# Performance work log

Hardware: AMD Instinct MI355X
Metric: run time of the kernel (lower is better)

## Reference

```python
import jax, jax.numpy as jnp
import numpy as np

B, S, D_IN, D_OUT = 4, 4096, 2048, 2048
DELTA_A = 0.0
DELTA_W = 0.05


def setup_inputs() -> dict:
    key = jax.random.key(0)
    kx, kw = jax.random.split(key)
    # xavier_uniform bound for [out, in] weight
    bound = float(np.sqrt(6.0 / (D_IN + D_OUT)))
    x = jax.random.normal(kx, (B, S, D_IN), dtype=jnp.float32)
    W = jax.random.uniform(kw, (D_OUT, D_IN), dtype=jnp.float32, minval=-bound, maxval=bound)
    b = jnp.zeros((D_OUT,), dtype=jnp.float32)
    return {"x": x, "W": W, "b": b}


def reference(x, W, b):
    # --- activation ternarization (BitNet STE); pre_ln=False -> identity ---
    ax = jnp.abs(x)
    thr_a = DELTA_A * jnp.mean(ax, axis=-1, keepdims=True)
    xa = jnp.where(ax < thr_a, jnp.zeros_like(x), jnp.sign(x))
    x_final = x + jax.lax.stop_gradient(xa - x)

    # --- weight ternarization with per-row alpha scale ---
    Wc = W - jnp.mean(W, axis=1, keepdims=True)
    aWc = jnp.abs(Wc)
    thr_w = DELTA_W * jnp.mean(aWc, axis=1, keepdims=True)
    code = jnp.where(aWc < thr_w, jnp.zeros_like(Wc), jnp.sign(Wc))
    nz = (code != 0).astype(Wc.dtype)
    alpha = jnp.sum(aWc * nz, axis=1, keepdims=True) / jnp.clip(
        jnp.sum(nz, axis=1, keepdims=True), 1.0, None
    )
    Wq = alpha * code
    W_final = W + jax.lax.stop_gradient(Wq - W)

    # F.linear: y = x @ W^T + b
    return jnp.einsum("bsd,od->bso", x_final, W_final) + b
```

## Files before the change

### kernel.cpp

```cpp
#include <hip/hip_runtime.h>
#include <stdint.h>

#define K_DIM   2048
#define N_DIM   2048
#define M_DIM   16384
#define DELTA_W 0.05f

#define BM 256
#define BN 256
#define BK 128
#define NT (K_DIM / BK)

typedef __attribute__((ext_vector_type(4))) int i32x4;

__device__ __forceinline__ void async_copy16(const void* g, void* l) {
    __builtin_amdgcn_global_load_lds(
        (__attribute__((address_space(1))) void*)g,
        (__attribute__((address_space(3))) void*)l,
        16, 0, 0);
}

__device__ __forceinline__ float block_sum_256(float v, float* sm) {
#pragma unroll
    for (int o = 32; o > 0; o >>= 1) v += __shfl_down(v, o, 64);
    const int lane = threadIdx.x & 63;
    const int w    = threadIdx.x >> 6;
    __syncthreads();
    if (lane == 0) sm[w] = v;
    __syncthreads();
    return sm[0] + sm[1] + sm[2] + sm[3];
}

__global__ __launch_bounds__(256) void quant_kernel(
    const float* __restrict__ W, const float* __restrict__ x,
    int8_t* __restrict__ code, float* __restrict__ alpha,
    int8_t* __restrict__ xq)
{
    __shared__ float sm[4];
    const int t = threadIdx.x;

    if (blockIdx.x < N_DIM) {
        const int row = blockIdx.x;
        const float* Wr = W + (size_t)row * K_DIM;

        float v[8];
        float s = 0.f;
#pragma unroll
        for (int i = 0; i < 8; ++i) { v[i] = Wr[t + i * 256]; s += v[i]; }
        const float mean = block_sum_256(s, sm) * (1.0f / K_DIM);

        float sa = 0.f;
#pragma unroll
        for (int i = 0; i < 8; ++i) sa += fabsf(v[i] - mean);
        const float thr = DELTA_W * (block_sum_256(sa, sm) * (1.0f / K_DIM));

        float ssum = 0.f, scnt = 0.f;
        int8_t q[8];
#pragma unroll
        for (int i = 0; i < 8; ++i) {
            const float c = v[i] - mean;
            const float a = fabsf(c);
            int8_t qv = 0;
            if (a >= thr) qv = (int8_t)((c > 0.f) - (c < 0.f));
            q[i] = qv;
            if (qv != 0) { ssum += a; scnt += 1.0f; }
        }
        const float num = block_sum_256(ssum, sm);
        const float den = block_sum_256(scnt, sm);
        if (t == 0) alpha[row] = num / fmaxf(den, 1.0f);

#pragma unroll
        for (int i = 0; i < 8; ++i)
            code[(size_t)row * K_DIM + t + i * 256] = q[i];
    } else {
        const int blk = blockIdx.x - N_DIM;
        const int base = blk * 1024 + t;
        const float4* xin = (const float4*)x;
        char4* xo = (char4*)xq;
#pragma unroll
        for (int i = 0; i < 4; ++i) {
            const float4 f = xin[base + i * 256];
            char4 c;
            c.x = (char)((f.x > 0.f) - (f.x < 0.f));
            c.y = (char)((f.y > 0.f) - (f.y < 0.f));
            c.z = (char)((f.z > 0.f) - (f.z < 0.f));
            c.w = (char)((f.w > 0.f) - (f.w < 0.f));
            xo[base + i * 256] = c;
        }
    }
}

__global__ __launch_bounds__(512) void gemm_kernel(
    const int8_t* __restrict__ A, const int8_t* __restrict__ Bt,
    const float* __restrict__ alpha, const float* __restrict__ bias,
    float* __restrict__ out)
{
    __shared__ __align__(16) int8_t As[2][BM * BK];
    __shared__ __align__(16) int8_t Bs[2][BN * BK];

    const int tid  = threadIdx.x;
    const int lane = tid & 63;
    const int wv   = tid >> 6;
    const int wm   = (wv >> 2) * 128;
    const int wn   = (wv & 3) * 64;
    const int fr   = lane & 15;
    const int q    = lane >> 4;
    const int c0   = q ^ (fr & 7);

    const int tileM = blockIdx.y * BM;
    const int tileN = blockIdx.x * BN;

    size_t a_src[2][2], b_src[2][2];
#pragma unroll
    for (int e = 0; e < 2; ++e) {
        const int s  = e * 512 + tid;
        const int r  = s >> 3;
        const int cg = (s & 7) ^ (r & 7);
#pragma unroll
        for (int h = 0; h < 2; ++h) {
            a_src[h][e] = (size_t)(tileM + h * 128 + r) * K_DIM + cg * 16;
            b_src[h][e] = (size_t)(tileN + h * 128 + r) * K_DIM + cg * 16;
        }
    }

    i32x4 acc[8][4] = {};
    i32x4 af[2][4], bf0[2][2], bf1[2][2];

#define STAGE_A(nbp, h, kk0) do {                                              \
    async_copy16(A  + a_src[h][0] + (kk0), &As[nbp][(h) * 16384 + tid * 16]);  \
    async_copy16(A  + a_src[h][1] + (kk0),                                     \
                 &As[nbp][(h) * 16384 + 8192 + tid * 16]);                     \
} while (0)
#define STAGE_B(nbp, h, kk0) do {                                              \
    async_copy16(Bt + b_src[h][0] + (kk0), &Bs[nbp][(h) * 16384 + tid * 16]);  \
    async_copy16(Bt + b_src[h][1] + (kk0),                                     \
                 &Bs[nbp][(h) * 16384 + 8192 + tid * 16]);                     \
} while (0)

    STAGE_A(0, 0, 0); STAGE_B(0, 0, 0);
    STAGE_B(0, 1, 0); STAGE_A(0, 1, 0);

    int k1 = 0;

#define GROUP(bp, DS, WV) {                                                    \
    const int8_t* Ac = As[(bp)];                                               \
    const int8_t* Bc = Bs[(bp)];                                               \
    const int nb = (bp) ^ 1;                                                   \
    if (DS) { STAGE_A(nb, 0, k1); STAGE_B(nb, 0, k1);                          \
              STAGE_B(nb, 1, k1); STAGE_A(nb, 1, k1); }                        \
    asm volatile("s_waitcnt vmcnt(" WV ")\n\ts_barrier" ::: "memory");         \
                               \
    _Pragma("unroll")                                                          \
    for (int i = 0; i < 4; ++i) {                                              \
        const int r8 = (wm + i * 16 + fr) * 128;                               \
        af[0][i] = *(const i32x4*)(Ac + r8 + c0 * 16);                         \
        af[1][i] = *(const i32x4*)(Ac + r8 + (c0 ^ 4) * 16);                   \
    }                                                                          \
    _Pragma("unroll")                                                          \
    for (int j = 0; j < 2; ++j) {                                              \
        const int r8a = (wn + j * 16 + fr) * 128;                              \
        bf0[0][j] = *(const i32x4*)(Bc + r8a + c0 * 16);                       \
        bf0[1][j] = *(const i32x4*)(Bc + r8a + (c0 ^ 4) * 16);                 \
        const int r8b = (wn + 32 + j * 16 + fr) * 128;                         \
        bf1[0][j] = *(const i32x4*)(Bc + r8b + c0 * 16);                       \
        bf1[1][j] = *(const i32x4*)(Bc + r8b + (c0 ^ 4) * 16);                 \
    }                                                                          \
                                    \
    _Pragma("unroll")                                                          \
    for (int i = 0; i < 4; ++i) {                                              \
        _Pragma("unroll")                                                      \
        for (int j = 0; j < 2; ++j) {                                          \
            acc[i][j] = __builtin_amdgcn_mfma_i32_16x16x64_i8(                 \
                af[0][i], bf0[0][j], acc[i][j], 0, 0, 0);                      \
            acc[i][j] = __builtin_amdgcn_mfma_i32_16x16x64_i8(                 \
                af[1][i], bf0[1][j], acc[i][j], 0, 0, 0);                      \
            acc[i][j + 2] = __builtin_amdgcn_mfma_i32_16x16x64_i8(             \
                af[0][i], bf1[0][j], acc[i][j + 2], 0, 0, 0);                  \
            acc[i][j + 2] = __builtin_amdgcn_mfma_i32_16x16x64_i8(             \
                af[1][i], bf1[1][j], acc[i][j + 2], 0, 0, 0);                  \
        }                                                                      \
    }                                                                          \
                      \
    _Pragma("unroll")                                                          \
    for (int i = 0; i < 4; ++i) {                                              \
        const int r8 = (wm + 64 + i * 16 + fr) * 128;                          \
        af[0][i] = *(const i32x4*)(Ac + r8 + c0 * 16);                         \
        af[1][i] = *(const i32x4*)(Ac + r8 + (c0 ^ 4) * 16);                   \
    }                                                                          \
                                    \
    _Pragma("unroll")                                                          \
    for (int i = 0; i < 4; ++i) {                                              \
        _Pragma("unroll")                                                      \
        for (int j = 0; j < 2; ++j) {                                          \
            acc[i + 4][j] = __builtin_amdgcn_mfma_i32_16x16x64_i8(             \
                af[0][i], bf0[0][j], acc[i + 4][j], 0, 0, 0);                  \
            acc[i + 4][j] = __builtin_amdgcn_mfma_i32_16x16x64_i8(             \
                af[1][i], bf0[1][j], acc[i + 4][j], 0, 0, 0);                  \
            acc[i + 4][j + 2] = __builtin_amdgcn_mfma_i32_16x16x64_i8(         \
                af[0][i], bf1[0][j], acc[i + 4][j + 2], 0, 0, 0);              \
            acc[i + 4][j + 2] = __builtin_amdgcn_mfma_i32_16x16x64_i8(         \
                af[1][i], bf1[1][j], acc[i + 4][j + 2], 0, 0, 0);              \
        }                                                                      \
    }                                                                          \
                    \
    asm volatile("s_barrier" ::: "memory");                                    \
}

#pragma unroll 1
    for (int t = 0; t < NT - 1; ++t) {
        k1 = (t + 1) * BK;
        GROUP(t & 1, 1, "8");
    }
    GROUP((NT - 1) & 1, 0, "0");

#undef GROUP
#undef STAGE_A
#undef STAGE_B

    const int cl = lane & 15;
    const int qr = lane >> 4;
#pragma unroll
    for (int j = 0; j < 4; ++j) {
        const int n  = tileN + wn + j * 16 + cl;
        const float al = alpha[n];
        const float bi = bias[n];
#pragma unroll
        for (int i = 0; i < 8; ++i) {
            const int mbase = tileM + wm + i * 16 + qr * 4;
#pragma unroll
            for (int r = 0; r < 4; ++r) {
                out[(size_t)(mbase + r) * N_DIM + n] =
                    al * (float)acc[i][j][r] + bi;
            }
        }
    }
}

extern "C" void kernel_launch(void* const* d_in, const int* in_sizes, int n_in,
                              void* d_out, int out_size, void* d_ws, size_t ws_size,
                              hipStream_t stream) {
    const float* x = (const float*)d_in[0];
    const float* W = (const float*)d_in[1];
    const float* b = (const float*)d_in[2];
    float* out = (float*)d_out;

    int8_t* xq    = (int8_t*)d_ws;
    int8_t* wcode = xq + (size_t)M_DIM * K_DIM;
    float*  alpha = (float*)(wcode + (size_t)N_DIM * K_DIM);

    quant_kernel<<<N_DIM + 8192, 256, 0, stream>>>(W, x, wcode, alpha, xq);

    dim3 grid(N_DIM / BN, M_DIM / BM);
    gemm_kernel<<<grid, dim3(512), 0, stream>>>(xq, wcode, alpha, b, out);
}
```

Before: 312.0 us.

## Restructure int8 GEMM main loop into ping-pong quadrant schedule with XCD-aware tile mapping

Splits each K tile into four MFMA quadrants separated by barriers, with lgkmcnt waits and s_setprio raised around the MFMA bursts. Global-to-LDS copies for the next buffer are issued partway through the current tile, and two tiles are prefetched up front. A 1D grid is remapped so each XCD handles a contiguous band of M tiles for better L2 reuse, and launch bounds request two blocks per CU. The aim is to overlap LDS reads, global loads and MFMA across waves. The cost is many more barriers, and two blocks of 512 threads with 128KB LDS each may not actually fit on a CU.

```diff
diff --git a/kernel.cpp b/kernel.cpp
--- a/kernel.cpp
+++ b/kernel.cpp
@@ -90,7 +90,7 @@
     }
 }
 
-__global__ __launch_bounds__(512) void gemm_kernel(
+__global__ __launch_bounds__(512, 2) void gemm_kernel(
     const int8_t* __restrict__ A, const int8_t* __restrict__ Bt,
     const float* __restrict__ alpha, const float* __restrict__ bias,
     float* __restrict__ out)
@@ -105,10 +105,13 @@
     const int wn   = (wv & 3) * 64;
     const int fr   = lane & 15;
     const int q    = lane >> 4;
-    const int c0   = q ^ (fr & 7);
-
-    const int tileM = blockIdx.y * BM;
-    const int tileN = blockIdx.x * BN;
+    const int x0   = (q ^ (fr & 7)) * 16;
+
+    const int bid = blockIdx.x;
+    const int xcd = bid & 7;
+    const int idx = bid >> 3;
+    const int tileN = (idx & 7) * BN;
+    const int tileM = ((idx >> 3) + xcd * 8) * BM;
 
     size_t a_src[2][2], b_src[2][2];
 #pragma unroll
@@ -126,96 +129,94 @@
     i32x4 acc[8][4] = {};
     i32x4 af[2][4], bf0[2][2], bf1[2][2];
 
-#define STAGE_A(nbp, h, kk0) do {                                              \
-    async_copy16(A  + a_src[h][0] + (kk0), &As[nbp][(h) * 16384 + tid * 16]);  \
+#define STAGE_A(D, h, kk0) do {                                                \
+    async_copy16(A  + a_src[h][0] + (kk0), &As[D][(h) * 16384 + tid * 16]);    \
     async_copy16(A  + a_src[h][1] + (kk0),                                     \
-                 &As[nbp][(h) * 16384 + 8192 + tid * 16]);                     \
+                 &As[D][(h) * 16384 + 8192 + tid * 16]);                       \
 } while (0)
-#define STAGE_B(nbp, h, kk0) do {                                              \
-    async_copy16(Bt + b_src[h][0] + (kk0), &Bs[nbp][(h) * 16384 + tid * 16]);  \
+#define STAGE_B(D, h, kk0) do {                                                \
+    async_copy16(Bt + b_src[h][0] + (kk0), &Bs[D][(h) * 16384 + tid * 16]);    \
     async_copy16(Bt + b_src[h][1] + (kk0),                                     \
-                 &Bs[nbp][(h) * 16384 + 8192 + tid * 16]);                     \
+                 &Bs[D][(h) * 16384 + 8192 + tid * 16]);                       \
 } while (0)
 
-    STAGE_A(0, 0, 0); STAGE_B(0, 0, 0);
-    STAGE_B(0, 1, 0); STAGE_A(0, 1, 0);
-
-    int k1 = 0;
-
-#define GROUP(bp, DS, WV) {                                                    \
-    const int8_t* Ac = As[(bp)];                                               \
-    const int8_t* Bc = Bs[(bp)];                                               \
-    const int nb = (bp) ^ 1;                                                   \
-    if (DS) { STAGE_A(nb, 0, k1); STAGE_B(nb, 0, k1);                          \
-              STAGE_B(nb, 1, k1); STAGE_A(nb, 1, k1); }                        \
-    asm volatile("s_waitcnt vmcnt(" WV ")\n\ts_barrier" ::: "memory");         \
-                               \
+#define BARRIER    asm volatile("s_barrier" ::: "memory")
+#define VMBAR(W)   asm volatile("s_waitcnt vmcnt(" W ")\n\ts_barrier" ::: "memory")
+#define LGKM0      do { asm volatile("s_waitcnt lgkmcnt(0)" ::: "memory");     \
+                        __builtin_amdgcn_sched_barrier(0); } while (0)
+#define PRIO1      __builtin_amdgcn_s_setprio(1)
+#define PRIO0      __builtin_amdgcn_s_setprio(0)
+
+#define RD_AF(Ap, MQ) {                                                        \
     _Pragma("unroll")                                                          \
     for (int i = 0; i < 4; ++i) {                                              \
-        const int r8 = (wm + i * 16 + fr) * 128;                               \
-        af[0][i] = *(const i32x4*)(Ac + r8 + c0 * 16);                         \
-        af[1][i] = *(const i32x4*)(Ac + r8 + (c0 ^ 4) * 16);                   \
+        const int r8 = (wm + (MQ) * 64 + i * 16 + fr) * 128;                   \
+        af[0][i] = *(const i32x4*)((Ap) + r8 + x0);                            \
+        af[1][i] = *(const i32x4*)((Ap) + r8 + (x0 ^ 64));                     \
     }                                                                          \
+}
+#define RD_BF(Bp, F, NQ) {                                                     \
     _Pragma("unroll")                                                          \
     for (int j = 0; j < 2; ++j) {                                              \
-        const int r8a = (wn + j * 16 + fr) * 128;                              \
-        bf0[0][j] = *(const i32x4*)(Bc + r8a + c0 * 16);                       \
-        bf0[1][j] = *(const i32x4*)(Bc + r8a + (c0 ^ 4) * 16);                 \
-        const int r8b = (wn + 32 + j * 16 + fr) * 128;                         \
-        bf1[0][j] = *(const i32x4*)(Bc + r8b + c0 * 16);                       \
-        bf1[1][j] = *(const i32x4*)(Bc + r8b + (c0 ^ 4) * 16);                 \
+        const int r8 = (wn + (NQ) * 32 + j * 16 + fr) * 128;                   \
+        F[0][j] = *(const i32x4*)((Bp) + r8 + x0);                             \
+        F[1][j] = *(const i32x4*)((Bp) + r8 + (x0 ^ 64));                      \
     }                                                                          \
-                                    \
+}
+#define MMQ(F, R, C) {                                                         \
     _Pragma("unroll")                                                          \
     for (int i = 0; i < 4; ++i) {                                              \
         _Pragma("unroll")                                                      \
         for (int j = 0; j < 2; ++j) {                                          \
-            acc[i][j] = __builtin_amdgcn_mfma_i32_16x16x64_i8(                 \
-                af[0][i], bf0[0][j], acc[i][j], 0, 0, 0);                      \
-            acc[i][j] = __builtin_amdgcn_mfma_i32_16x16x64_i8(                 \
-                af[1][i], bf0[1][j], acc[i][j], 0, 0, 0);                      \
-            acc[i][j + 2] = __builtin_amdgcn_mfma_i32_16x16x64_i8(             \
-                af[0][i], bf1[0][j], acc[i][j + 2], 0, 0, 0);                  \
-            acc[i][j + 2] = __builtin_amdgcn_mfma_i32_16x16x64_i8(             \
-                af[1][i], bf1[1][j], acc[i][j + 2], 0, 0, 0);                  \
+            acc[(R) + i][(C) + j] = __builtin_amdgcn_mfma_i32_16x16x64_i8(     \
+                af[0][i], F[0][j], acc[(R) + i][(C) + j], 0, 0, 0);            \
+            acc[(R) + i][(C) + j] = __builtin_amdgcn_mfma_i32_16x16x64_i8(     \
+                af[1][i], F[1][j], acc[(R) + i][(C) + j], 0, 0, 0);            \
         }                                                                      \
     }                                                                          \
+}
+
+#define KTILE(Ap, Bp, D, DS, KN, W) {                                          \
+                                                             \
+    RD_AF(Ap, 0); RD_BF(Bp, bf0, 0);                                           \
+    BARRIER; LGKM0; PRIO1; MMQ(bf0, 0, 0); PRIO0; BARRIER;                     \
+                                                             \
+    RD_BF(Bp, bf1, 1);                                                         \
+    BARRIER; LGKM0; PRIO1; MMQ(bf1, 0, 2); PRIO0; BARRIER;                     \
+                                                   \
+    RD_AF(Ap, 1);                                                              \
+    if (DS) { STAGE_B(D, 0, KN); STAGE_B(D, 1, KN); }                          \
+    BARRIER; LGKM0; PRIO1; MMQ(bf1, 4, 2); PRIO0; BARRIER;                     \
                       \
-    _Pragma("unroll")                                                          \
-    for (int i = 0; i < 4; ++i) {                                              \
-        const int r8 = (wm + 64 + i * 16 + fr) * 128;                          \
-        af[0][i] = *(const i32x4*)(Ac + r8 + c0 * 16);                         \
-        af[1][i] = *(const i32x4*)(Ac + r8 + (c0 ^ 4) * 16);                   \
-    }                                                                          \
-                                    \
-    _Pragma("unroll")                                                          \
-    for (int i = 0; i < 4; ++i) {                                              \
-        _Pragma("unroll")                                                      \
-        for (int j = 0; j < 2; ++j) {                                          \
-            acc[i + 4][j] = __builtin_amdgcn_mfma_i32_16x16x64_i8(             \
-                af[0][i], bf0[0][j], acc[i + 4][j], 0, 0, 0);                  \
-            acc[i + 4][j] = __builtin_amdgcn_mfma_i32_16x16x64_i8(             \
-                af[1][i], bf0[1][j], acc[i + 4][j], 0, 0, 0);                  \
-            acc[i + 4][j + 2] = __builtin_amdgcn_mfma_i32_16x16x64_i8(         \
-                af[0][i], bf1[0][j], acc[i + 4][j + 2], 0, 0, 0);              \
-            acc[i + 4][j + 2] = __builtin_amdgcn_mfma_i32_16x16x64_i8(         \
-                af[1][i], bf1[1][j], acc[i + 4][j + 2], 0, 0, 0);              \
-        }                                                                      \
-    }                                                                          \
-                    \
-    asm volatile("s_barrier" ::: "memory");                                    \
-}
+    if (DS) { STAGE_A(D, 0, KN); STAGE_A(D, 1, KN); }                          \
+    BARRIER; LGKM0; PRIO1; MMQ(bf0, 4, 0); PRIO0; VMBAR(W);                    \
+}
+
+    STAGE_A(0, 0, 0); STAGE_A(0, 1, 0); STAGE_B(0, 0, 0); STAGE_B(0, 1, 0);
+    STAGE_A(1, 0, BK); STAGE_A(1, 1, BK); STAGE_B(1, 0, BK); STAGE_B(1, 1, BK);
+    VMBAR("8");
 
 #pragma unroll 1
-    for (int t = 0; t < NT - 1; ++t) {
-        k1 = (t + 1) * BK;
-        GROUP(t & 1, 1, "8");
-    }
-    GROUP((NT - 1) & 1, 0, "0");
-
-#undef GROUP
+    for (int it = 0; it < NT / 2 - 1; ++it) {
+        const int kn0 = (2 * it + 2) * BK;
+        const int kn1 = (2 * it + 3) * BK;
+        KTILE((const int8_t*)As[0], (const int8_t*)Bs[0], 0, 1, kn0, "8");
+        KTILE((const int8_t*)As[1], (const int8_t*)Bs[1], 1, 1, kn1, "8");
+    }
+    KTILE((const int8_t*)As[0], (const int8_t*)Bs[0], 0, 0, 0, "0");
+    KTILE((const int8_t*)As[1], (const int8_t*)Bs[1], 1, 0, 0, "0");
+
+#undef KTILE
+#undef MMQ
+#undef RD_BF
+#undef RD_AF
+#undef PRIO0
+#undef PRIO1
+#undef LGKM0
+#undef VMBAR
+#undef BARRIER
+#undef STAGE_B
 #undef STAGE_A
-#undef STAGE_B
 
     const int cl = lane & 15;
     const int qr = lane >> 4;
@@ -250,6 +251,5 @@
 
     quant_kernel<<<N_DIM + 8192, 256, 0, stream>>>(W, x, wcode, alpha, xq);
 
-    dim3 grid(N_DIM / BN, M_DIM / BM);
-    gemm_kernel<<<grid, dim3(512), 0, stream>>>(xq, wcode, alpha, b, out);
-}
+    gemm_kernel<<<512, dim3(512), 0, stream>>>(xq, wcode, alpha, b, out);
+}
```

Result: faster. 305.7 us (-2.0%).
